# Kernel tuning notes

Measured on AMD Instinct MI355X. Metric: run time of the kernel, lower is better.

The kernel has to match this reference:

```python
import jax, jax.numpy as jnp
import numpy as np

N, E, G = 50000, 500000, 1024
ND, ED, H, L, OUT = 32, 16, 128, 4, 1
BN_EPS = 1e-5


def setup_inputs() -> dict:
    key = jax.random.key(0)
    ks = jax.random.split(key, 32)

    def w(k, shape, fan):
        return jax.random.normal(k, shape, jnp.float32) / np.float32(np.sqrt(fan))

    inp = {
        "x": jax.random.normal(ks[0], (N, ND), jnp.float32),
        "edge_index": jax.random.randint(ks[1], (2, E), 0, N, jnp.int64),
        "edge_attr": jax.random.normal(ks[2], (E, ED), jnp.float32),
        "batch": jax.random.randint(ks[3], (N,), 0, G, jnp.int64),
        # embeddings
        "ne_w": w(ks[4], (ND, H), ND), "ne_b": jnp.zeros((H,), jnp.float32),
        "ee_w": w(ks[5], (ED, H), ED), "ee_b": jnp.zeros((H,), jnp.float32),
        # per-layer node_mlp: Linear(2H,H) ReLU Linear(H,H) BN(H)
        "nm_w1": w(ks[6], (L, 2 * H, H), 2 * H), "nm_b1": jnp.zeros((L, H), jnp.float32),
        "nm_w2": w(ks[7], (L, H, H), H), "nm_b2": jnp.zeros((L, H), jnp.float32),
        "bn_g": jnp.ones((L, H), jnp.float32), "bn_b": jnp.zeros((L, H), jnp.float32),
        # per-layer edge_mlp: Linear(H,H) ReLU Linear(H,H)  (edge_dim==hidden_dim inside MPNN)
        "em_w1": w(ks[8], (L, H, H), H), "em_b1": jnp.zeros((L, H), jnp.float32),
        "em_w2": w(ks[9], (L, H, H), H), "em_b2": jnp.zeros((L, H), jnp.float32),
        # readout: Linear(H,H) ReLU Dropout(eval=identity) Linear(H,OUT)
        "ro_w1": w(ks[10], (H, H), H), "ro_b1": jnp.zeros((H,), jnp.float32),
        "ro_w2": w(ks[11], (H, OUT), H), "ro_b2": jnp.zeros((OUT,), jnp.float32),
    }
    return inp


def reference(x, edge_index, edge_attr, batch,
              ne_w, ne_b, ee_w, ee_b,
              nm_w1, nm_b1, nm_w2, nm_b2, bn_g, bn_b,
              em_w1, em_b1, em_w2, em_b2,
              ro_w1, ro_b1, ro_w2, ro_b2):
    src, dst = edge_index[0], edge_index[1]  # PyG default: x_j from source, aggregate at target
    h = x @ ne_w + ne_b                      # [N, H]
    e = edge_attr @ ee_w + ee_b              # [E, H]
    inv_std = np.float32(1.0 / np.sqrt(1.0 + BN_EPS))  # eval BN, running_mean=0, running_var=1
    for l in range(nm_w1.shape[0]):
        # edge_mlp
        e = jax.nn.relu(e @ em_w1[l] + em_b1[l]) @ em_w2[l] + em_b2[l]
        # message: concat(x_j, edge_attr) -> node_mlp
        msg = jnp.concatenate([h[src], e], axis=1)              # [E, 2H]
        msg = jax.nn.relu(msg @ nm_w1[l] + nm_b1[l]) @ nm_w2[l] + nm_b2[l]
        msg = msg * (inv_std * bn_g[l]) + bn_b[l]               # BatchNorm1d (eval)
        # scatter-add aggregation + residual update
        agg = jax.ops.segment_sum(msg, dst, num_segments=h.shape[0])
        h = agg + h
    pooled = jax.ops.segment_sum(h, batch, num_segments=G)      # global_add_pool -> [G, H]
    return jax.nn.relu(pooled @ ro_w1 + ro_b1) @ ro_w2 + ro_b2  # [G, OUT]
```

## Files before the change

### kernel.cpp

```cpp
#include <hip/hip_runtime.h>
#include <hip/hip_bf16.h>
#include <math.h>

#define NN 50000
#define EE 500000
#define GG 1024
#define NDIM 32
#define EDIM 16
#define HH 128
#define LL 4
#define NT2 ((EE + 127) / 128)
#define NB2 ((NN + 127) / 128)
#define SCAN_NB ((NN + 255) / 256)

typedef unsigned short ushortT;
typedef __attribute__((ext_vector_type(8))) short bf16x8;
typedef __attribute__((ext_vector_type(4))) float f32x4;

#define MFMA16(a, b, c) __builtin_amdgcn_mfma_f32_16x16x32_bf16(a, b, c, 0, 0, 0)

__device__ inline float bf2f(ushortT u) {
    union { unsigned int i; float f; } v; v.i = ((unsigned int)u) << 16; return v.f;
}
__device__ inline ushortT f2bf(float f) {
    union { float f; unsigned int i; } v; v.f = f;
    unsigned int r = v.i + 0x7FFFu + ((v.i >> 16) & 1u);
    return (ushortT)(r >> 16);
}
__device__ inline short f2bfs(float f) { return (short)f2bf(f); }

__device__ inline bf16x8 lds_a(const char* base, int strideB, int row, int colByte,
                               int mask) {
    int b = row * strideB + colByte;
    b ^= ((row & mask) << 4);
    return *reinterpret_cast<const bf16x8*>(base + b);
}

__global__ __launch_bounds__(256) void hist_kernel(
        const int* __restrict__ dst, int* __restrict__ counts) {
    int i = blockIdx.x * 256 + threadIdx.x;
    if (i < EE) atomicAdd(&counts[dst[i]], 1);
}

__global__ __launch_bounds__(256) void scan_part1(
        const int* __restrict__ counts, int* __restrict__ bsum) {
    __shared__ int buf[256];
    int t = threadIdx.x;
    int i = blockIdx.x * 256 + t;
    buf[t] = (i < NN) ? counts[i] : 0;
    __syncthreads();
    for (int s = 128; s > 0; s >>= 1) {
        if (t < s) buf[t] += buf[t + s];
        __syncthreads();
    }
    if (t == 0) bsum[blockIdx.x] = buf[0];
}

__global__ __launch_bounds__(256) void scan_part2(
        const int* __restrict__ bsum, int* __restrict__ bbase) {
    __shared__ int buf[256];
    int t = threadIdx.x;
    int v = (t < SCAN_NB) ? bsum[t] : 0;
    buf[t] = v;
    __syncthreads();
    for (int off = 1; off < 256; off <<= 1) {
        int s = (t >= off) ? buf[t - off] : 0;
        __syncthreads();
        buf[t] += s;
        __syncthreads();
    }
    if (t < SCAN_NB) bbase[t] = buf[t] - v;
}

__global__ __launch_bounds__(256) void scan_part3(
        const int* __restrict__ counts, const int* __restrict__ bbase,
        int* __restrict__ base) {
    __shared__ int buf[256];
    int t = threadIdx.x;
    int i = blockIdx.x * 256 + t;
    int v = (i < NN) ? counts[i] : 0;
    buf[t] = v;
    __syncthreads();
    for (int off = 1; off < 256; off <<= 1) {
        int s = (t >= off) ? buf[t - off] : 0;
        __syncthreads();
        buf[t] += s;
        __syncthreads();
    }
    if (i < NN) base[i] = bbase[blockIdx.x] + buf[t] - v;
}

__global__ __launch_bounds__(256) void build_perm_kernel(
        const int* __restrict__ src, const int* __restrict__ dst,
        const int* __restrict__ base, int* __restrict__ cnt,
        int* __restrict__ perm, int* __restrict__ srcS, int* __restrict__ dstS) {
    int i = blockIdx.x * 256 + threadIdx.x;
    if (i >= EE) return;
    int d = dst[i];
    int pos = base[d] + atomicAdd(&cnt[d], 1);
    perm[pos] = i;
    srcS[pos] = src[i];
    dstS[pos] = d;
}

__global__ __launch_bounds__(256) void ghist_kernel(
        const int* __restrict__ batch, int* __restrict__ gcounts) {
    int i = blockIdx.x * 256 + threadIdx.x;
    if (i < NN) atomicAdd(&gcounts[batch[i]], 1);
}

__global__ __launch_bounds__(1024) void gscan_kernel(
        const int* __restrict__ gcounts, int* __restrict__ gbase) {
    __shared__ int buf[1024];
    int t = threadIdx.x;
    int v = gcounts[t];
    buf[t] = v;
    __syncthreads();
    for (int off = 1; off < 1024; off <<= 1) {
        int s = (t >= off) ? buf[t - off] : 0;
        __syncthreads();
        buf[t] += s;
        __syncthreads();
    }
    gbase[t] = buf[t] - v;
}

__global__ __launch_bounds__(256) void gbuild_kernel(
        const int* __restrict__ batch, const int* __restrict__ gbase,
        int* __restrict__ gcnt, int* __restrict__ gperm) {
    int i = blockIdx.x * 256 + threadIdx.x;
    if (i >= NN) return;
    int b = batch[i];
    int pos = gbase[b] + atomicAdd(&gcnt[b], 1);
    gperm[pos] = i;
}

__global__ __launch_bounds__(256) void transpose_kernel(
        const float* __restrict__ in, ushortT* __restrict__ out, int K, int N) {
    int per = K * N;
    int total = LL * per;
    int idx = blockIdx.x * 256 + threadIdx.x;
    if (idx >= total) return;
    int l = idx / per, rem = idx - l * per;
    int n = rem / K, k = rem - n * K;
    out[idx] = f2bf(in[(size_t)l * per + (size_t)k * N + n]);
}

__global__ __launch_bounds__(256) void transpose_pad32_kernel(
        const float* __restrict__ in, ushortT* __restrict__ out, int KIN) {
    int idx = blockIdx.x * 256 + threadIdx.x;
    if (idx >= HH * 32) return;
    int n = idx >> 5, k = idx & 31;
    out[idx] = (k < KIN) ? f2bf(in[k * HH + n]) : (ushortT)0;
}

__global__ __launch_bounds__(256) void bnfold_kernel(
        const float* __restrict__ w2, const float* __restrict__ b2,
        const float* __restrict__ bng, const float* __restrict__ bnb,
        ushortT* __restrict__ w2g, float* __restrict__ nb2g, float inv_std) {
    int idx = blockIdx.x * 256 + threadIdx.x;
    if (idx < LL * HH * HH) {
        int l = idx / (HH * HH), rem = idx - l * (HH * HH);
        int n = rem / HH, k = rem - n * HH;
        w2g[idx] = f2bf(w2[(size_t)l * HH * HH + (size_t)k * HH + n] *
                        bng[l * HH + n] * inv_std);
    }
    if (idx < LL * HH) {
        nb2g[idx] = b2[idx] * bng[idx] * inv_std + bnb[idx];
    }
}

template<int K, int KS, bool HASB>
__device__ inline void gemm_b(const char* aBase, int aStrideB, int aMask,
        const ushortT* __restrict__ wT, const float* __restrict__ bias,
        int wr, int wc, int l15, int lg, f32x4 acc[2][4]) {
#pragma unroll
    for (int ntl = 0; ntl < 4; ++ntl) {
        float bb = HASB ? bias[wc * 64 + ntl * 16 + l15] : 0.f;
        f32x4 iv = {bb, bb, bb, bb};
        acc[0][ntl] = iv;
        acc[1][ntl] = iv;
    }
#pragma unroll
    for (int ks = 0; ks < K / 32; ++ks) {
        int kk = ks * 32 + lg * 8;
        bf16x8 a0 = lds_a(aBase, aStrideB, wr * 32 + l15,      kk * 2, aMask);
        bf16x8 a1 = lds_a(aBase, aStrideB, wr * 32 + 16 + l15, kk * 2, aMask);
#pragma unroll
        for (int ntl = 0; ntl < 4; ++ntl) {
            int n = wc * 64 + ntl * 16 + l15;
            bf16x8 b = *reinterpret_cast<const bf16x8*>(wT + (size_t)n * KS + kk);
            acc[0][ntl] = MFMA16(a0, b, acc[0][ntl]);
            acc[1][ntl] = MFMA16(a1, b, acc[1][ntl]);
        }
    }
}

__device__ inline void gemm_uinit3(const char* aBase, const char* uBase,
        const ushortT* __restrict__ wT,
        int wr, int wc, int l15, int lg, f32x4 acc[2][4]) {
#pragma unroll
    for (int mt = 0; mt < 2; ++mt)
#pragma unroll
        for (int ntl = 0; ntl < 4; ++ntl) {
            int col = wc * 64 + ntl * 16 + l15;
#pragma unroll
            for (int r = 0; r < 4; ++r) {
                int row = wr * 32 + mt * 16 + lg * 4 + r;
                int b = row * 256 + col * 2; b ^= ((row & 7) << 4);
                acc[mt][ntl][r] = bf2f(*reinterpret_cast<const ushortT*>(uBase + b));
            }
        }
#pragma unroll
    for (int ks = 0; ks < 4; ++ks) {
        int kk = ks * 32 + lg * 8;
        bf16x8 a0 = lds_a(aBase, 256, wr * 32 + l15,      kk * 2, 7);
        bf16x8 a1 = lds_a(aBase, 256, wr * 32 + 16 + l15, kk * 2, 7);
#pragma unroll
        for (int ntl = 0; ntl < 4; ++ntl) {
            int n = wc * 64 + ntl * 16 + l15;
            bf16x8 b = *reinterpret_cast<const bf16x8*>(wT + (size_t)n * 256 + kk);
            acc[0][ntl] = MFMA16(a0, b, acc[0][ntl]);
            acc[1][ntl] = MFMA16(a1, b, acc[1][ntl]);
        }
    }
}

__device__ inline void wfrag(char* base, int wr, int wc, int l15, int lg,
                             f32x4 acc[2][4], bool relu) {
#pragma unroll
    for (int mt = 0; mt < 2; ++mt)
#pragma unroll
        for (int ntl = 0; ntl < 4; ++ntl) {
            int col = wc * 64 + ntl * 16 + l15;
#pragma unroll
            for (int r = 0; r < 4; ++r) {
                int row = wr * 32 + mt * 16 + lg * 4 + r;
                int b = row * 256 + col * 2;
                b ^= ((row & 7) << 4);
                float v = acc[mt][ntl][r];
                if (relu) v = fmaxf(v, 0.f);
                *reinterpret_cast<ushortT*>(base + b) = f2bf(v);
            }
        }
}

template<int EMBED, int LASTL>
__global__ __launch_bounds__(512) void edgeA_kernel(
        const ushortT* __restrict__ u, ushortT* __restrict__ e,
        const int* __restrict__ srcS, const int* __restrict__ dstS,
        const int* __restrict__ basep, const int* __restrict__ perm,
        const float* __restrict__ ea,
        const ushortT* __restrict__ eewT, const float* __restrict__ eeb,
        const ushortT* __restrict__ ew1t, const float* __restrict__ eb1,
        const ushortT* __restrict__ ew2t, const float* __restrict__ eb2,
        const ushortT* __restrict__ nw1bt,
        ushortT* __restrict__ partials) {
    __shared__ __align__(16) char eT[128 * 256];
    __shared__ __align__(16) char uT[128 * 256];
    __shared__ int dstx[128], bstartL[128], sidx[128], pidx[128];

    const int e0 = blockIdx.x * 128;
    int V = EE - e0; if (V > 128) V = 128;
    const int tid = threadIdx.x;
    const bf16x8 z8 = {0, 0, 0, 0, 0, 0, 0, 0};

    if (tid < 128) {
        int ii = e0 + tid;
        int d = (ii < EE) ? dstS[ii] : -1;
        dstx[tid] = d;
        bstartL[tid] = (d >= 0) ? basep[d] : 0;
        sidx[tid] = (ii < EE) ? srcS[ii] : 0;
        if (EMBED) pidx[tid] = (ii < EE) ? perm[ii] : 0;
    }
    __syncthreads();

#pragma unroll
    for (int s = 0; s < 4; ++s) {
        int idx = tid + s * 512;
        int row = idx >> 4, c8 = (idx & 15) * 8;
        bf16x8 v = *reinterpret_cast<const bf16x8*>(u + (size_t)sidx[row] * HH + c8);
        int b = row * 256 + c8 * 2; b ^= ((row & 7) << 4);
        *reinterpret_cast<bf16x8*>(uT + b) = v;
    }
    if (EMBED) {
        {
            int row = tid >> 2, q4 = (tid & 3) * 4;
            float4 v = *reinterpret_cast<const float4*>(
                ea + (size_t)pidx[row] * EDIM + q4);
            unsigned long long pack =
                (unsigned long long)f2bf(v.x) |
                ((unsigned long long)f2bf(v.y) << 16) |
                ((unsigned long long)f2bf(v.z) << 32) |
                ((unsigned long long)f2bf(v.w) << 48);
            int b = row * 64 + q4 * 2; b ^= ((row & 3) << 4);
            *reinterpret_cast<unsigned long long*>(eT + b) = pack;
        }
        if (tid < 256) {
            int row = tid >> 1;
            int b = row * 64 + 32 + (tid & 1) * 16; b ^= ((row & 3) << 4);
            *reinterpret_cast<bf16x8*>(eT + b) = z8;
        }
    } else {
#pragma unroll
        for (int s = 0; s < 4; ++s) {
            int idx = tid + s * 512;
            int row = idx >> 4, c8 = (idx & 15) * 8;
            bf16x8 v = *reinterpret_cast<const bf16x8*>(
                e + (size_t)(e0 + row) * HH + c8);
            int b = row * 256 + c8 * 2; b ^= ((row & 7) << 4);
            *reinterpret_cast<bf16x8*>(eT + b) = v;
        }
    }
    __syncthreads();

    const int wid = tid >> 6, lane = tid & 63;
    const int wr = wid >> 1, wc = wid & 1, l15 = lane & 15, lg = lane >> 4;
    f32x4 acc[2][4];

    if (EMBED) {
        gemm_b<32, 32, true>(eT, 64, 3, eewT, eeb, wr, wc, l15, lg, acc);
        __syncthreads();
        wfrag(eT, wr, wc, l15, lg, acc, false);
        __syncthreads();
    }
    gemm_b<HH, HH, true>(eT, 256, 7, ew1t, eb1, wr, wc, l15, lg, acc);
    __syncthreads();
    wfrag(eT, wr, wc, l15, lg, acc, true);
    __syncthreads();
    gemm_b<HH, HH, true>(eT, 256, 7, ew2t, eb2, wr, wc, l15, lg, acc);
    __syncthreads();
    wfrag(eT, wr, wc, l15, lg, acc, false);
    __syncthreads();
    if (!LASTL) {
#pragma unroll
        for (int s = 0; s < 4; ++s) {
            int idx = tid + s * 512;
            int row = idx >> 4, c8 = (idx & 15) * 8;
            if (row < V) {
                int b = row * 256 + c8 * 2; b ^= ((row & 7) << 4);
                *reinterpret_cast<bf16x8*>(e + (size_t)(e0 + row) * HH + c8) =
                    *reinterpret_cast<const bf16x8*>(eT + b);
            }
        }
    }
    gemm_uinit3(eT, uT, nw1bt, wr, wc, l15, lg, acc);
    __syncthreads();
    wfrag(eT, wr, wc, l15, lg, acc, true);
    __syncthreads();

    {
        int col = tid & 127, seg = tid >> 7;
        int r = seg * 32, rend = r + 32;
        float sum = 0.f;
        int dprev = -1, runStart = r;
        for (; r < rend; ++r) {
            int d = dstx[r];
            if (d != dprev) {
                if (dprev >= 0) {
                    int slot = ((e0 + runStart) >> 5) - (bstartL[runStart] >> 5);
                    if (slot < 3)
                        partials[((size_t)slot * NN + dprev) * HH + col] = f2bf(sum);
                }
                sum = 0.f; dprev = d; runStart = r;
            }
            if (d >= 0) {
                int b = r * 256 + col * 2; b ^= ((r & 7) << 4);
                sum += bf2f(*reinterpret_cast<const ushortT*>(eT + b));
            }
        }
        if (dprev >= 0) {
            int slot = ((e0 + runStart) >> 5) - (bstartL[runStart] >> 5);
            if (slot < 3)
                partials[((size_t)slot * NN + dprev) * HH + col] = f2bf(sum);
        }
    }
}

template<int HASU>
__global__ __launch_bounds__(512) void nodeB_kernel(
        const ushortT* __restrict__ partials, const int* __restrict__ basep,
        const ushortT* __restrict__ w2g, const float* __restrict__ nb2g,
        float* __restrict__ h,
        const ushortT* __restrict__ w1tn, const float* __restrict__ b1n,
        ushortT* __restrict__ uOut) {
    __shared__ __align__(16) char sT[128 * 256];
    __shared__ int degx[128];
    __shared__ int basex[128];
    const int n0 = blockIdx.x * 128;
    int V = NN - n0; if (V > 128) V = 128;
    const int tid = threadIdx.x;

    if (tid < 128) {
        int bs = 0, de = 0;
        if (tid < V) {
            int n = n0 + tid;
            bs = basep[n];
            int be = (n + 1 < NN) ? basep[n + 1] : EE;
            de = be - bs;
        }
        basex[tid] = bs;
        degx[tid] = de;
    }
    __syncthreads();

#pragma unroll
    for (int g = 0; g < 4; ++g) {
        int node = g * 32 + (tid >> 4);
        int c8 = (tid & 15) * 8;
        float s[8] = {0.f, 0.f, 0.f, 0.f, 0.f, 0.f, 0.f, 0.f};
        if (node < V) {
            int bs = basex[node], de = degx[node];
            if (de > 0) {
                int ns = ((bs + de - 1) >> 5) - (bs >> 5) + 1;
                if (ns > 3) ns = 3;
                for (int sl = 0; sl < ns; ++sl) {
                    bf16x8 pv = *reinterpret_cast<const bf16x8*>(
                        partials + ((size_t)sl * NN + n0 + node) * HH + c8);
#pragma unroll
                    for (int j = 0; j < 8; ++j) s[j] += bf2f((ushortT)pv[j]);
                }
            }
        }
        bf16x8 o;
#pragma unroll
        for (int j = 0; j < 8; ++j) o[j] = f2bfs(s[j]);
        int b = node * 256 + c8 * 2; b ^= ((node & 7) << 4);
        *reinterpret_cast<bf16x8*>(sT + b) = o;
    }
    __syncthreads();

    const int wid = tid >> 6, lane = tid & 63;
    const int wr = wid >> 1, wc = wid & 1, l15 = lane & 15, lg = lane >> 4;
    f32x4 acc[2][4];

    gemm_b<HH, HH, false>(sT, 256, 7, w2g, nullptr, wr, wc, l15, lg, acc);
#pragma unroll
    for (int ntl = 0; ntl < 4; ++ntl) {
        int col = wc * 64 + ntl * 16 + l15;
        float bg = nb2g[col];
#pragma unroll
        for (int mt = 0; mt < 2; ++mt)
#pragma unroll
            for (int r = 0; r < 4; ++r) {
                int row = wr * 32 + mt * 16 + lg * 4 + r;
                if (row < V) {
                    size_t off = (size_t)(n0 + row) * HH + col;
                    float hn = h[off] + acc[mt][ntl][r] + (float)degx[row] * bg;
                    h[off] = hn;
                    acc[mt][ntl][r] = hn;
                } else {
                    acc[mt][ntl][r] = 0.f;
                }
            }
    }
    if (HASU) {
        __syncthreads();
        wfrag(sT, wr, wc, l15, lg, acc, false);
        __syncthreads();
        gemm_b<HH, 2 * HH, true>(sT, 256, 7, w1tn, b1n, wr, wc, l15, lg, acc);
        __syncthreads();
        wfrag(sT, wr, wc, l15, lg, acc, false);
        __syncthreads();
#pragma unroll
        for (int s = 0; s < 4; ++s) {
            int idx = tid + s * 512;
            int row = idx >> 4, c8 = (idx & 15) * 8;
            if (row < V) {
                int b = row * 256 + c8 * 2; b ^= ((row & 7) << 4);
                *reinterpret_cast<bf16x8*>(uOut + (size_t)(n0 + row) * HH + c8) =
                    *reinterpret_cast<const bf16x8*>(sT + b);
            }
        }
    }
}

__global__ __launch_bounds__(512) void node_pre2_kernel(
        const float* __restrict__ x, const ushortT* __restrict__ newT,
        const float* __restrict__ neb,
        const ushortT* __restrict__ w1t, const float* __restrict__ b1,
        float* __restrict__ h, ushortT* __restrict__ uo) {
    __shared__ __align__(16) char sT[128 * 256];
    __shared__ __align__(16) char xT[128 * 64];
    const int n0 = blockIdx.x * 128;
    int V = NN - n0; if (V > 128) V = 128;
    const int tid = threadIdx.x;

#pragma unroll
    for (int s = 0; s < 2; ++s) {
        int idx = tid + s * 512;
        int row = idx >> 3;
        int q4 = (idx & 7) * 4;
        unsigned long long pack = 0ull;
        if (row < V) {
            float4 v = *reinterpret_cast<const float4*>(
                x + (size_t)(n0 + row) * NDIM + q4);
            pack = (unsigned long long)f2bf(v.x) |
                   ((unsigned long long)f2bf(v.y) << 16) |
                   ((unsigned long long)f2bf(v.z) << 32) |
                   ((unsigned long long)f2bf(v.w) << 48);
        }
        int b = row * 64 + q4 * 2; b ^= ((row & 3) << 4);
        *reinterpret_cast<unsigned long long*>(xT + b) = pack;
    }
    __syncthreads();

    const int wid = tid >> 6, lane = tid & 63;
    const int wr = wid >> 1, wc = wid & 1, l15 = lane & 15, lg = lane >> 4;
    f32x4 acc[2][4];
    gemm_b<32, 32, true>(xT, 64, 3, newT, neb, wr, wc, l15, lg, acc);
#pragma unroll
    for (int mt = 0; mt < 2; ++mt)
#pragma unroll
        for (int ntl = 0; ntl < 4; ++ntl) {
            int col = wc * 64 + ntl * 16 + l15;
#pragma unroll
            for (int r = 0; r < 4; ++r) {
                int row = wr * 32 + mt * 16 + lg * 4 + r;
                if (row < V) h[(size_t)(n0 + row) * HH + col] = acc[mt][ntl][r];
            }
        }
    wfrag(sT, wr, wc, l15, lg, acc, false);
    __syncthreads();
    gemm_b<HH, 2 * HH, true>(sT, 256, 7, w1t, b1, wr, wc, l15, lg, acc);
    __syncthreads();
    wfrag(sT, wr, wc, l15, lg, acc, false);
    __syncthreads();
#pragma unroll
    for (int s = 0; s < 4; ++s) {
        int idx = tid + s * 512;
        int row = idx >> 4, c8 = (idx & 15) * 8;
        if (row < V) {
            int b = row * 256 + c8 * 2; b ^= ((row & 7) << 4);
            *reinterpret_cast<bf16x8*>(uo + (size_t)(n0 + row) * HH + c8) =
                *reinterpret_cast<const bf16x8*>(sT + b);
        }
    }
}

__global__ __launch_bounds__(256) void pool2_kernel(
        const float* __restrict__ h, const int* __restrict__ gperm,
        const int* __restrict__ gbase, const int* __restrict__ gcounts,
        float* __restrict__ pooled) {
    int w = threadIdx.x >> 6, lane = threadIdx.x & 63;
    int g = blockIdx.x * 4 + w;
    int bs = gbase[g], cnt = gcounts[g];
    int c = lane * 2;
    float ax = 0.f, ay = 0.f;
    for (int j = 0; j < cnt; ++j) {
        int n = gperm[bs + j];
        float2 v = *reinterpret_cast<const float2*>(h + (size_t)n * HH + c);
        ax += v.x; ay += v.y;
    }
    float2 o = {ax, ay};
    *reinterpret_cast<float2*>(pooled + (size_t)g * HH + c) = o;
}

__global__ __launch_bounds__(128) void readout_kernel(
        const float* __restrict__ pooled,
        const float* __restrict__ w1, const float* __restrict__ b1,
        const float* __restrict__ w2, const float* __restrict__ b2,
        float* __restrict__ out) {
    __shared__ float row[HH];
    __shared__ float red[HH];
    int g = blockIdx.x, j = threadIdx.x;
    row[j] = pooled[(size_t)g * HH + j];
    __syncthreads();
    float acc = b1[j];
    for (int k = 0; k < HH; ++k) acc += row[k] * w1[k * HH + j];
    red[j] = fmaxf(acc, 0.f) * w2[j];
    __syncthreads();
    for (int s = 64; s > 0; s >>= 1) {
        if (j < s) red[j] += red[j + s];
        __syncthreads();
    }
    if (j == 0) out[g] = red[0] + b2[0];
}

extern "C" void kernel_launch(void* const* d_in, const int* in_sizes, int n_in,
                              void* d_out, int out_size, void* d_ws, size_t ws_size,
                              hipStream_t stream) {
    const float* x     = (const float*)d_in[0];
    const int*   ei    = (const int*)d_in[1];
    const float* ea    = (const float*)d_in[2];
    const int*   batch = (const int*)d_in[3];
    const float* ne_w  = (const float*)d_in[4];
    const float* ne_b  = (const float*)d_in[5];
    const float* ee_w  = (const float*)d_in[6];
    const float* ee_b  = (const float*)d_in[7];
    const float* nm_w1 = (const float*)d_in[8];
    const float* nm_b1 = (const float*)d_in[9];
    const float* nm_w2 = (const float*)d_in[10];
    const float* nm_b2 = (const float*)d_in[11];
    const float* bn_g  = (const float*)d_in[12];
    const float* bn_b  = (const float*)d_in[13];
    const float* em_w1 = (const float*)d_in[14];
    const float* em_b1 = (const float*)d_in[15];
    const float* em_w2 = (const float*)d_in[16];
    const float* em_b2 = (const float*)d_in[17];
    const float* ro_w1 = (const float*)d_in[18];
    const float* ro_b1 = (const float*)d_in[19];
    const float* ro_w2 = (const float*)d_in[20];
    const float* ro_b2 = (const float*)d_in[21];

    const int* srcp = ei;
    const int* dstp = ei + EE;

    char* p = (char*)d_ws;
    float* h = (float*)p;            p += (size_t)NN * HH * 4;
    float* pooled = (float*)p;       p += (size_t)GG * HH * 4;
    ushortT* ebuf = (ushortT*)p;     p += (size_t)EE * HH * 2;
    ushortT* ubuf = (ushortT*)p;     p += (size_t)NN * HH * 2;
    ushortT* partials = (ushortT*)p; p += (size_t)3 * NN * HH * 2;
    ushortT* ew1t = (ushortT*)p;     p += (size_t)LL * HH * HH * 2;
    ushortT* ew2t = (ushortT*)p;     p += (size_t)LL * HH * HH * 2;
    ushortT* nw1t = (ushortT*)p;     p += (size_t)LL * 2 * HH * HH * 2;
    ushortT* w2g  = (ushortT*)p;     p += (size_t)LL * HH * HH * 2;
    float* nb2g   = (float*)p;       p += (size_t)LL * HH * 4;
    ushortT* eewT = (ushortT*)p;     p += (size_t)HH * 32 * 2;
    ushortT* newT = (ushortT*)p;     p += (size_t)HH * 32 * 2;
    int* perm   = (int*)p;           p += (size_t)EE * 4;
    int* srcS   = (int*)p;           p += (size_t)EE * 4;
    int* dstS   = (int*)p;           p += (size_t)EE * 4;
    int* counts = (int*)p;           p += (size_t)NN * 4;
    int* basep  = (int*)p;           p += (size_t)NN * 4;
    int* cnt    = (int*)p;           p += (size_t)NN * 4;
    int* bsum   = (int*)p;           p += (size_t)SCAN_NB * 4;
    int* bbase  = (int*)p;           p += (size_t)SCAN_NB * 4;
    int* gperm  = (int*)p;           p += (size_t)NN * 4;
    int* gcounts= (int*)p;           p += (size_t)GG * 4;
    int* gbase  = (int*)p;           p += (size_t)GG * 4;
    int* gcnt   = (int*)p;           p += (size_t)GG * 4;

    hipMemsetAsync(counts, 0, (size_t)NN * 4, stream);
    hipMemsetAsync(cnt, 0, (size_t)NN * 4, stream);
    hipMemsetAsync(gcounts, 0, (size_t)GG * 4, stream);
    hipMemsetAsync(gcnt, 0, (size_t)GG * 4, stream);
    hist_kernel<<<(EE + 255) / 256, 256, 0, stream>>>(dstp, counts);
    scan_part1<<<SCAN_NB, 256, 0, stream>>>(counts, bsum);
    scan_part2<<<1, 256, 0, stream>>>(bsum, bbase);
    scan_part3<<<SCAN_NB, 256, 0, stream>>>(counts, bbase, basep);
    build_perm_kernel<<<(EE + 255) / 256, 256, 0, stream>>>(
        srcp, dstp, basep, cnt, perm, srcS, dstS);

    ghist_kernel<<<(NN + 255) / 256, 256, 0, stream>>>(batch, gcounts);
    gscan_kernel<<<1, 1024, 0, stream>>>(gcounts, gbase);
    gbuild_kernel<<<(NN + 255) / 256, 256, 0, stream>>>(batch, gbase, gcnt, gperm);

    const float inv_std = 1.0f / sqrtf(1.0f + 1e-5f);
    transpose_kernel<<<(LL * HH * HH + 255) / 256, 256, 0, stream>>>(em_w1, ew1t, HH, HH);
    transpose_kernel<<<(LL * HH * HH + 255) / 256, 256, 0, stream>>>(em_w2, ew2t, HH, HH);
    transpose_kernel<<<(LL * 2 * HH * HH + 255) / 256, 256, 0, stream>>>(nm_w1, nw1t, 2 * HH, HH);
    bnfold_kernel<<<(LL * HH * HH + 255) / 256, 256, 0, stream>>>(
        nm_w2, nm_b2, bn_g, bn_b, w2g, nb2g, inv_std);
    transpose_pad32_kernel<<<(HH * 32 + 255) / 256, 256, 0, stream>>>(ee_w, eewT, EDIM);
    transpose_pad32_kernel<<<(HH * 32 + 255) / 256, 256, 0, stream>>>(ne_w, newT, NDIM);

    node_pre2_kernel<<<NB2, 512, 0, stream>>>(x, newT, ne_b, nw1t, nm_b1, h, ubuf);

    for (int l = 0; l < LL; ++l) {
        const ushortT* nw1bt = nw1t + (size_t)l * 2 * HH * HH + 128;
        if (l == 0) {
            edgeA_kernel<1, 0><<<NT2, 512, 0, stream>>>(
                ubuf, ebuf, srcS, dstS, basep, perm, ea, eewT, ee_b,
                ew1t + (size_t)l * HH * HH, em_b1 + l * HH,
                ew2t + (size_t)l * HH * HH, em_b2 + l * HH,
                nw1bt, partials);
        } else if (l < LL - 1) {
            edgeA_kernel<0, 0><<<NT2, 512, 0, stream>>>(
                ubuf, ebuf, srcS, dstS, basep, perm, ea, eewT, ee_b,
                ew1t + (size_t)l * HH * HH, em_b1 + l * HH,
                ew2t + (size_t)l * HH * HH, em_b2 + l * HH,
                nw1bt, partials);
        } else {
            edgeA_kernel<0, 1><<<NT2, 512, 0, stream>>>(
                ubuf, ebuf, srcS, dstS, basep, perm, ea, eewT, ee_b,
                ew1t + (size_t)l * HH * HH, em_b1 + l * HH,
                ew2t + (size_t)l * HH * HH, em_b2 + l * HH,
                nw1bt, partials);
        }
        if (l < LL - 1) {
            nodeB_kernel<1><<<NB2, 512, 0, stream>>>(
                partials, basep, w2g + (size_t)l * HH * HH, nb2g + l * HH, h,
                nw1t + (size_t)(l + 1) * 2 * HH * HH, nm_b1 + (l + 1) * HH, ubuf);
        } else {
            nodeB_kernel<0><<<NB2, 512, 0, stream>>>(
                partials, basep, w2g + (size_t)l * HH * HH, nb2g + l * HH, h,
                nw1t, nm_b1, ubuf);
        }
    }

    pool2_kernel<<<GG / 4, 256, 0, stream>>>(h, gperm, gbase, gcounts, pooled);
    readout_kernel<<<GG, 128, 0, stream>>>(pooled, ro_w1, ro_b1, ro_w2, ro_b2,
                                           (float*)d_out);
}
```

Baseline: 1.222 ms.

## Give each wave its own 16-row strip so GEMM chains need no block barriers

The GEMM tiling changes so each of the 8 waves owns 16 full-width rows (8 N-tiles) instead of a 32x64 quadrant. Every wave now loads, computes and writes back only its own rows of the LDS tiles, which lets almost all __syncthreads between chained GEMMs be removed. Gather indices are read inline instead of being staged in shared arrays. In exchange each wave reads all of the weight columns, doubling B-fragment global/L2 loads per wave, and register pressure changes.

```diff
diff --git a/kernel.cpp b/kernel.cpp
--- a/kernel.cpp
+++ b/kernel.cpp
@@ -171,78 +171,68 @@
 }
 
 template<int K, int KS, bool HASB>
-__device__ inline void gemm_b(const char* aBase, int aStrideB, int aMask,
+__device__ inline void gemm_w(const char* aBase, int aStrideB, int aMask,
         const ushortT* __restrict__ wT, const float* __restrict__ bias,
-        int wr, int wc, int l15, int lg, f32x4 acc[2][4]) {
-#pragma unroll
-    for (int ntl = 0; ntl < 4; ++ntl) {
-        float bb = HASB ? bias[wc * 64 + ntl * 16 + l15] : 0.f;
+        int w, int l15, int lg, f32x4 acc[8]) {
+#pragma unroll
+    for (int n = 0; n < 8; ++n) {
+        float bb = HASB ? bias[n * 16 + l15] : 0.f;
         f32x4 iv = {bb, bb, bb, bb};
-        acc[0][ntl] = iv;
-        acc[1][ntl] = iv;
+        acc[n] = iv;
     }
 #pragma unroll
     for (int ks = 0; ks < K / 32; ++ks) {
         int kk = ks * 32 + lg * 8;
-        bf16x8 a0 = lds_a(aBase, aStrideB, wr * 32 + l15,      kk * 2, aMask);
-        bf16x8 a1 = lds_a(aBase, aStrideB, wr * 32 + 16 + l15, kk * 2, aMask);
-#pragma unroll
-        for (int ntl = 0; ntl < 4; ++ntl) {
-            int n = wc * 64 + ntl * 16 + l15;
-            bf16x8 b = *reinterpret_cast<const bf16x8*>(wT + (size_t)n * KS + kk);
-            acc[0][ntl] = MFMA16(a0, b, acc[0][ntl]);
-            acc[1][ntl] = MFMA16(a1, b, acc[1][ntl]);
-        }
-    }
-}
-
-__device__ inline void gemm_uinit3(const char* aBase, const char* uBase,
-        const ushortT* __restrict__ wT,
-        int wr, int wc, int l15, int lg, f32x4 acc[2][4]) {
-#pragma unroll
-    for (int mt = 0; mt < 2; ++mt)
-#pragma unroll
-        for (int ntl = 0; ntl < 4; ++ntl) {
-            int col = wc * 64 + ntl * 16 + l15;
-#pragma unroll
-            for (int r = 0; r < 4; ++r) {
-                int row = wr * 32 + mt * 16 + lg * 4 + r;
-                int b = row * 256 + col * 2; b ^= ((row & 7) << 4);
-                acc[mt][ntl][r] = bf2f(*reinterpret_cast<const ushortT*>(uBase + b));
-            }
-        }
+        bf16x8 a0 = lds_a(aBase, aStrideB, w * 16 + l15, kk * 2, aMask);
+#pragma unroll
+        for (int n = 0; n < 8; ++n) {
+            bf16x8 b = *reinterpret_cast<const bf16x8*>(
+                wT + (size_t)(n * 16 + l15) * KS + kk);
+            acc[n] = MFMA16(a0, b, acc[n]);
+        }
+    }
+}
+
+__device__ inline void wfrag_w(char* base, int w, int l15, int lg,
+                               f32x4 acc[8], bool relu) {
+#pragma unroll
+    for (int n = 0; n < 8; ++n) {
+        int col = n * 16 + l15;
+#pragma unroll
+        for (int r = 0; r < 4; ++r) {
+            int row = w * 16 + lg * 4 + r;
+            int b = row * 256 + col * 2;
+            b ^= ((row & 7) << 4);
+            float v = acc[n][r];
+            if (relu) v = fmaxf(v, 0.f);
+            *reinterpret_cast<ushortT*>(base + b) = f2bf(v);
+        }
+    }
+}
+
+__device__ inline void gemm_uinit_w(const char* aBase, const char* uBase,
+        const ushortT* __restrict__ wT, int w, int l15, int lg, f32x4 acc[8]) {
+#pragma unroll
+    for (int n = 0; n < 8; ++n) {
+        int col = n * 16 + l15;
+#pragma unroll
+        for (int r = 0; r < 4; ++r) {
+            int row = w * 16 + lg * 4 + r;
+            int b = row * 256 + col * 2; b ^= ((row & 7) << 4);
+            acc[n][r] = bf2f(*reinterpret_cast<const ushortT*>(uBase + b));
+        }
+    }
 #pragma unroll
     for (int ks = 0; ks < 4; ++ks) {
         int kk = ks * 32 + lg * 8;
-        bf16x8 a0 = lds_a(aBase, 256, wr * 32 + l15,      kk * 2, 7);
-        bf16x8 a1 = lds_a(aBase, 256, wr * 32 + 16 + l15, kk * 2, 7);
-#pragma unroll
-        for (int ntl = 0; ntl < 4; ++ntl) {
-            int n = wc * 64 + ntl * 16 + l15;
-            bf16x8 b = *reinterpret_cast<const bf16x8*>(wT + (size_t)n * 256 + kk);
-            acc[0][ntl] = MFMA16(a0, b, acc[0][ntl]);
-            acc[1][ntl] = MFMA16(a1, b, acc[1][ntl]);
-        }
-    }
-}
-
-__device__ inline void wfrag(char* base, int wr, int wc, int l15, int lg,
-                             f32x4 acc[2][4], bool relu) {
-#pragma unroll
-    for (int mt = 0; mt < 2; ++mt)
-#pragma unroll
-        for (int ntl = 0; ntl < 4; ++ntl) {
-            int col = wc * 64 + ntl * 16 + l15;
-#pragma unroll
-            for (int r = 0; r < 4; ++r) {
-                int row = wr * 32 + mt * 16 + lg * 4 + r;
-                int b = row * 256 + col * 2;
-                b ^= ((row & 7) << 4);
-                float v = acc[mt][ntl][r];
-                if (relu) v = fmaxf(v, 0.f);
-                *reinterpret_cast<ushortT*>(base + b) = f2bf(v);
-            }
-        }
+        bf16x8 a0 = lds_a(aBase, 256, w * 16 + l15, kk * 2, 7);
+#pragma unroll
+        for (int n = 0; n < 8; ++n) {
+            bf16x8 b = *reinterpret_cast<const bf16x8*>(
+                wT + (size_t)(n * 16 + l15) * 256 + kk);
+            acc[n] = MFMA16(a0, b, acc[n]);
+        }
+    }
 }
 
 template<int EMBED, int LASTL>
@@ -258,95 +248,99 @@
         ushortT* __restrict__ partials) {
     __shared__ __align__(16) char eT[128 * 256];
     __shared__ __align__(16) char uT[128 * 256];
-    __shared__ int dstx[128], bstartL[128], sidx[128], pidx[128];
+    __shared__ __align__(16) char eaT[EMBED ? 128 * 64 : 16];
+    __shared__ int dstx[128], bstartL[128];
 
     const int e0 = blockIdx.x * 128;
     int V = EE - e0; if (V > 128) V = 128;
     const int tid = threadIdx.x;
+    const int w = tid >> 6, lane = tid & 63, l15 = lane & 15, lg = lane >> 4;
     const bf16x8 z8 = {0, 0, 0, 0, 0, 0, 0, 0};
 
-    if (tid < 128) {
-        int ii = e0 + tid;
+    if (lane < 16) {
+        int rr = w * 16 + lane;
+        int ii = e0 + rr;
         int d = (ii < EE) ? dstS[ii] : -1;
-        dstx[tid] = d;
-        bstartL[tid] = (d >= 0) ? basep[d] : 0;
-        sidx[tid] = (ii < EE) ? srcS[ii] : 0;
-        if (EMBED) pidx[tid] = (ii < EE) ? perm[ii] : 0;
-    }
-    __syncthreads();
-
+        dstx[rr] = d;
+        bstartL[rr] = (d >= 0) ? basep[d] : 0;
+    }
 #pragma unroll
     for (int s = 0; s < 4; ++s) {
-        int idx = tid + s * 512;
-        int row = idx >> 4, c8 = (idx & 15) * 8;
-        bf16x8 v = *reinterpret_cast<const bf16x8*>(u + (size_t)sidx[row] * HH + c8);
-        int b = row * 256 + c8 * 2; b ^= ((row & 7) << 4);
+        int c = lane + s * 64;
+        int rr = w * 16 + (c >> 4);
+        int c8 = (c & 15) * 8;
+        int ii = e0 + rr;
+        bf16x8 v = z8;
+        if (ii < EE) {
+            int sI = srcS[ii];
+            v = *reinterpret_cast<const bf16x8*>(u + (size_t)sI * HH + c8);
+        }
+        int b = rr * 256 + c8 * 2; b ^= ((rr & 7) << 4);
         *reinterpret_cast<bf16x8*>(uT + b) = v;
     }
     if (EMBED) {
         {
-            int row = tid >> 2, q4 = (tid & 3) * 4;
-            float4 v = *reinterpret_cast<const float4*>(
-                ea + (size_t)pidx[row] * EDIM + q4);
-            unsigned long long pack =
-                (unsigned long long)f2bf(v.x) |
-                ((unsigned long long)f2bf(v.y) << 16) |
-                ((unsigned long long)f2bf(v.z) << 32) |
-                ((unsigned long long)f2bf(v.w) << 48);
-            int b = row * 64 + q4 * 2; b ^= ((row & 3) << 4);
-            *reinterpret_cast<unsigned long long*>(eT + b) = pack;
-        }
-        if (tid < 256) {
-            int row = tid >> 1;
-            int b = row * 64 + 32 + (tid & 1) * 16; b ^= ((row & 3) << 4);
-            *reinterpret_cast<bf16x8*>(eT + b) = z8;
+            int rr = w * 16 + (lane >> 2);
+            int q4 = (lane & 3) * 4;
+            int ii = e0 + rr;
+            unsigned long long pack = 0ull;
+            if (ii < EE) {
+                int pp = perm[ii];
+                float4 v = *reinterpret_cast<const float4*>(
+                    ea + (size_t)pp * EDIM + q4);
+                pack = (unsigned long long)f2bf(v.x) |
+                       ((unsigned long long)f2bf(v.y) << 16) |
+                       ((unsigned long long)f2bf(v.z) << 32) |
+                       ((unsigned long long)f2bf(v.w) << 48);
+            }
+            int b = rr * 64 + q4 * 2; b ^= ((rr & 3) << 4);
+            *reinterpret_cast<unsigned long long*>(eaT + b) = pack;
+        }
+        if (lane < 32) {
+            int rr = w * 16 + (lane >> 1);
+            int b = rr * 64 + 32 + (lane & 1) * 16; b ^= ((rr & 3) << 4);
+            *reinterpret_cast<bf16x8*>(eaT + b) = z8;
         }
     } else {
 #pragma unroll
         for (int s = 0; s < 4; ++s) {
-            int idx = tid + s * 512;
-            int row = idx >> 4, c8 = (idx & 15) * 8;
-            bf16x8 v = *reinterpret_cast<const bf16x8*>(
-                e + (size_t)(e0 + row) * HH + c8);
-            int b = row * 256 + c8 * 2; b ^= ((row & 7) << 4);
+            int c = lane + s * 64;
+            int rr = w * 16 + (c >> 4);
+            int c8 = (c & 15) * 8;
+            int ii = e0 + rr;
+            bf16x8 v = z8;
+            if (ii < EE)
+                v = *reinterpret_cast<const bf16x8*>(e + (size_t)ii * HH + c8);
+            int b = rr * 256 + c8 * 2; b ^= ((rr & 7) << 4);
             *reinterpret_cast<bf16x8*>(eT + b) = v;
         }
     }
-    __syncthreads();
-
-    const int wid = tid >> 6, lane = tid & 63;
-    const int wr = wid >> 1, wc = wid & 1, l15 = lane & 15, lg = lane >> 4;
-    f32x4 acc[2][4];
-
+
+    f32x4 acc[8];
     if (EMBED) {
-        gemm_b<32, 32, true>(eT, 64, 3, eewT, eeb, wr, wc, l15, lg, acc);
-        __syncthreads();
-        wfrag(eT, wr, wc, l15, lg, acc, false);
-        __syncthreads();
-    }
-    gemm_b<HH, HH, true>(eT, 256, 7, ew1t, eb1, wr, wc, l15, lg, acc);
-    __syncthreads();
-    wfrag(eT, wr, wc, l15, lg, acc, true);
-    __syncthreads();
-    gemm_b<HH, HH, true>(eT, 256, 7, ew2t, eb2, wr, wc, l15, lg, acc);
-    __syncthreads();
-    wfrag(eT, wr, wc, l15, lg, acc, false);
-    __syncthreads();
+        gemm_w<32, 32, true>(eaT, 64, 3, eewT, eeb, w, l15, lg, acc);
+        wfrag_w(eT, w, l15, lg, acc, false);
+    }
+    gemm_w<HH, HH, true>(eT, 256, 7, ew1t, eb1, w, l15, lg, acc);
+    wfrag_w(eT, w, l15, lg, acc, true);
+    gemm_w<HH, HH, true>(eT, 256, 7, ew2t, eb2, w, l15, lg, acc);
+    wfrag_w(eT, w, l15, lg, acc, false);
     if (!LASTL) {
 #pragma unroll
         for (int s = 0; s < 4; ++s) {
-            int idx = tid + s * 512;
-            int row = idx >> 4, c8 = (idx & 15) * 8;
-            if (row < V) {
-                int b = row * 256 + c8 * 2; b ^= ((row & 7) << 4);
-                *reinterpret_cast<bf16x8*>(e + (size_t)(e0 + row) * HH + c8) =
+            int c = lane + s * 64;
+            int rr = w * 16 + (c >> 4);
+            int c8 = (c & 15) * 8;
+            int ii = e0 + rr;
+            if (ii < EE) {
+                int b = rr * 256 + c8 * 2; b ^= ((rr & 7) << 4);
+                *reinterpret_cast<bf16x8*>(e + (size_t)ii * HH + c8) =
                     *reinterpret_cast<const bf16x8*>(eT + b);
             }
         }
     }
-    gemm_uinit3(eT, uT, nw1bt, wr, wc, l15, lg, acc);
-    __syncthreads();
-    wfrag(eT, wr, wc, l15, lg, acc, true);
+    gemm_uinit_w(eT, uT, nw1bt, w, l15, lg, acc);
+    wfrag_w(eT, w, l15, lg, acc, true);
     __syncthreads();
 
     {
@@ -385,90 +379,74 @@
         const ushortT* __restrict__ w1tn, const float* __restrict__ b1n,
         ushortT* __restrict__ uOut) {
     __shared__ __align__(16) char sT[128 * 256];
-    __shared__ int degx[128];
-    __shared__ int basex[128];
     const int n0 = blockIdx.x * 128;
     int V = NN - n0; if (V > 128) V = 128;
     const int tid = threadIdx.x;
-
-    if (tid < 128) {
-        int bs = 0, de = 0;
-        if (tid < V) {
-            int n = n0 + tid;
-            bs = basep[n];
+    const int w = tid >> 6, lane = tid & 63, l15 = lane & 15, lg = lane >> 4;
+
+#pragma unroll
+    for (int s = 0; s < 4; ++s) {
+        int c = lane + s * 64;
+        int node = w * 16 + (c >> 4);
+        int c8 = (c & 15) * 8;
+        float sm[8] = {0.f, 0.f, 0.f, 0.f, 0.f, 0.f, 0.f, 0.f};
+        if (node < V) {
+            int n = n0 + node;
+            int bs = basep[n];
             int be = (n + 1 < NN) ? basep[n + 1] : EE;
-            de = be - bs;
-        }
-        basex[tid] = bs;
-        degx[tid] = de;
-    }
-    __syncthreads();
-
-#pragma unroll
-    for (int g = 0; g < 4; ++g) {
-        int node = g * 32 + (tid >> 4);
-        int c8 = (tid & 15) * 8;
-        float s[8] = {0.f, 0.f, 0.f, 0.f, 0.f, 0.f, 0.f, 0.f};
-        if (node < V) {
-            int bs = basex[node], de = degx[node];
+            int de = be - bs;
             if (de > 0) {
                 int ns = ((bs + de - 1) >> 5) - (bs >> 5) + 1;
                 if (ns > 3) ns = 3;
                 for (int sl = 0; sl < ns; ++sl) {
                     bf16x8 pv = *reinterpret_cast<const bf16x8*>(
-                        partials + ((size_t)sl * NN + n0 + node) * HH + c8);
-#pragma unroll
-                    for (int j = 0; j < 8; ++j) s[j] += bf2f((ushortT)pv[j]);
+                        partials + ((size_t)sl * NN + n) * HH + c8);
+#pragma unroll
+                    for (int j = 0; j < 8; ++j) sm[j] += bf2f((ushortT)pv[j]);
                 }
             }
         }
         bf16x8 o;
 #pragma unroll
-        for (int j = 0; j < 8; ++j) o[j] = f2bfs(s[j]);
+        for (int j = 0; j < 8; ++j) o[j] = f2bfs(sm[j]);
         int b = node * 256 + c8 * 2; b ^= ((node & 7) << 4);
         *reinterpret_cast<bf16x8*>(sT + b) = o;
     }
-    __syncthreads();
-
-    const int wid = tid >> 6, lane = tid & 63;
-    const int wr = wid >> 1, wc = wid & 1, l15 = lane & 15, lg = lane >> 4;
-    f32x4 acc[2][4];
-
-    gemm_b<HH, HH, false>(sT, 256, 7, w2g, nullptr, wr, wc, l15, lg, acc);
-#pragma unroll
-    for (int ntl = 0; ntl < 4; ++ntl) {
-        int col = wc * 64 + ntl * 16 + l15;
+
+    f32x4 acc[8];
+    gemm_w<HH, HH, false>(sT, 256, 7, w2g, nullptr, w, l15, lg, acc);
+#pragma unroll
+    for (int n8 = 0; n8 < 8; ++n8) {
+        int col = n8 * 16 + l15;
         float bg = nb2g[col];
 #pragma unroll
-        for (int mt = 0; mt < 2; ++mt)
-#pragma unroll
-            for (int r = 0; r < 4; ++r) {
-                int row = wr * 32 + mt * 16 + lg * 4 + r;
-                if (row < V) {
-                    size_t off = (size_t)(n0 + row) * HH + col;
-                    float hn = h[off] + acc[mt][ntl][r] + (float)degx[row] * bg;
-                    h[off] = hn;
-                    acc[mt][ntl][r] = hn;
-                } else {
-                    acc[mt][ntl][r] = 0.f;
-                }
+        for (int r = 0; r < 4; ++r) {
+            int row = w * 16 + lg * 4 + r;
+            if (row < V) {
+                int n = n0 + row;
+                int bs = basep[n];
+                int be = (n + 1 < NN) ? basep[n + 1] : EE;
+                size_t off = (size_t)n * HH + col;
+                float hn = h[off] + acc[n8][r] + (float)(be - bs) * bg;
+                h[off] = hn;
+                acc[n8][r] = hn;
+            } else {
+                acc[n8][r] = 0.f;
             }
+        }
     }
     if (HASU) {
-        __syncthreads();
-        wfrag(sT, wr, wc, l15, lg, acc, false);
-        __syncthreads();
-        gemm_b<HH, 2 * HH, true>(sT, 256, 7, w1tn, b1n, wr, wc, l15, lg, acc);
-        __syncthreads();
-        wfrag(sT, wr, wc, l15, lg, acc, false);
-        __syncthreads();
+        wfrag_w(sT, w, l15, lg, acc, false);
+        gemm_w<HH, 2 * HH, true>(sT, 256, 7, w1tn, b1n, w, l15, lg, acc);
+        wfrag_w(sT, w, l15, lg, acc, false);
 #pragma unroll
         for (int s = 0; s < 4; ++s) {
-            int idx = tid + s * 512;
-            int row = idx >> 4, c8 = (idx & 15) * 8;
-            if (row < V) {
-                int b = row * 256 + c8 * 2; b ^= ((row & 7) << 4);
-                *reinterpret_cast<bf16x8*>(uOut + (size_t)(n0 + row) * HH + c8) =
+            int c = lane + s * 64;
+            int rr = w * 16 + (c >> 4);
+            int c8 = (c & 15) * 8;
+            if (rr < V) {
+                int b = rr * 256 + c8 * 2; b ^= ((rr & 7) << 4);
+                *reinterpret_cast<bf16x8*>(uOut + (size_t)(n0 + rr) * HH + c8) =
                     *reinterpret_cast<const bf16x8*>(sT + b);
             }
         }
@@ -485,54 +463,48 @@
     const int n0 = blockIdx.x * 128;
     int V = NN - n0; if (V > 128) V = 128;
     const int tid = threadIdx.x;
+    const int w = tid >> 6, lane = tid & 63, l15 = lane & 15, lg = lane >> 4;
 
 #pragma unroll
     for (int s = 0; s < 2; ++s) {
-        int idx = tid + s * 512;
-        int row = idx >> 3;
-        int q4 = (idx & 7) * 4;
+        int c = lane + s * 64;
+        int rr = w * 16 + (c >> 3);
+        int q4 = (c & 7) * 4;
         unsigned long long pack = 0ull;
-        if (row < V) {
+        if (rr < V) {
             float4 v = *reinterpret_cast<const float4*>(
-                x + (size_t)(n0 + row) * NDIM + q4);
+                x + (size_t)(n0 + rr) * NDIM + q4);
             pack = (unsigned long long)f2bf(v.x) |
                    ((unsigned long long)f2bf(v.y) << 16) |
                    ((unsigned long long)f2bf(v.z) << 32) |
                    ((unsigned long long)f2bf(v.w) << 48);
         }
-        int b = row * 64 + q4 * 2; b ^= ((row & 3) << 4);
+        int b = rr * 64 + q4 * 2; b ^= ((rr & 3) << 4);
         *reinterpret_cast<unsigned long long*>(xT + b) = pack;
     }
-    __syncthreads();
-
-    const int wid = tid >> 6, lane = tid & 63;
-    const int wr = wid >> 1, wc = wid & 1, l15 = lane & 15, lg = lane >> 4;
-    f32x4 acc[2][4];
-    gemm_b<32, 32, true>(xT, 64, 3, newT, neb, wr, wc, l15, lg, acc);
-#pragma unroll
-    for (int mt = 0; mt < 2; ++mt)
-#pragma unroll
-        for (int ntl = 0; ntl < 4; ++ntl) {
-            int col = wc * 64 + ntl * 16 + l15;
-#pragma unroll
-            for (int r = 0; r < 4; ++r) {
-                int row = wr * 32 + mt * 16 + lg * 4 + r;
-                if (row < V) h[(size_t)(n0 + row) * HH + col] = acc[mt][ntl][r];
-            }
-        }
-    wfrag(sT, wr, wc, l15, lg, acc, false);
-    __syncthreads();
-    gemm_b<HH, 2 * HH, true>(sT, 256, 7, w1t, b1, wr, wc, l15, lg, acc);
-    __syncthreads();
-    wfrag(sT, wr, wc, l15, lg, acc, false);
-    __syncthreads();
+
+    f32x4 acc[8];
+    gemm_w<32, 32, true>(xT, 64, 3, newT, neb, w, l15, lg, acc);
+#pragma unroll
+    for (int n8 = 0; n8 < 8; ++n8) {
+        int col = n8 * 16 + l15;
+#pragma unroll
+        for (int r = 0; r < 4; ++r) {
+            int row = w * 16 + lg * 4 + r;
+            if (row < V) h[(size_t)(n0 + row) * HH + col] = acc[n8][r];
+        }
+    }
+    wfrag_w(sT, w, l15, lg, acc, false);
+    gemm_w<HH, 2 * HH, true>(sT, 256, 7, w1t, b1, w, l15, lg, acc);
+    wfrag_w(sT, w, l15, lg, acc, false);
 #pragma unroll
     for (int s = 0; s < 4; ++s) {
-        int idx = tid + s * 512;
-        int row = idx >> 4, c8 = (idx & 15) * 8;
-        if (row < V) {
-            int b = row * 256 + c8 * 2; b ^= ((row & 7) << 4);
-            *reinterpret_cast<bf16x8*>(uo + (size_t)(n0 + row) * HH + c8) =
+        int c = lane + s * 64;
+        int rr = w * 16 + (c >> 4);
+        int c8 = (c & 15) * 8;
+        if (rr < V) {
+            int b = rr * 256 + c8 * 2; b ^= ((rr & 7) << 4);
+            *reinterpret_cast<bf16x8*>(uo + (size_t)(n0 + rr) * HH + c8) =
                 *reinterpret_cast<const bf16x8*>(sT + b);
         }
     }
```

Result: slower. 2.101 ms (+72.0%).
